# Kernel tuning notes

Hardware: AMD Instinct MI355X
Metric: run time of the kernel (lower is better)

Reference implementation:

```python
import jax, jax.numpy as jnp
import numpy as np

B, L, H, G = 16, 1024, 1024, 128


def setup_inputs() -> dict:
    key = jax.random.key(0)
    ks = jax.random.split(key, 6)
    s = 0.02
    return {
        "events": jax.random.normal(ks[0], (B, L, H), jnp.float32),
        "contexts": jax.random.normal(ks[1], (B, L - 1, H), jnp.float32),
        "Wzm": jax.random.normal(ks[2], (2 * H, G), jnp.float32) * s,
        "bzm": jnp.zeros((G,), jnp.float32),
        "Wzv": jax.random.normal(ks[3], (2 * H, G), jnp.float32) * s,
        "bzv": jnp.zeros((G,), jnp.float32),
        "Wqm": jax.random.normal(ks[4], (3 * H, G), jnp.float32) * s,
        "bqm": jnp.zeros((G,), jnp.float32),
        "Wqv": jax.random.normal(ks[5], (3 * H, G), jnp.float32) * s,
        "bqv": jnp.zeros((G,), jnp.float32),
    }


def reference(events, contexts, Wzm, bzm, Wzv, bzv, Wqm, bqm, Wqv, bqv):
    # adjacent event pairs: [B, L-1, 2H]
    ep = jnp.concatenate([events[:, :-1, :], events[:, 1:, :]], axis=-1)
    z_mean = ep @ Wzm + bzm          # [B, L-1, G]
    z_log_var = ep @ Wzv + bzv
    ce = jnp.concatenate([ep, contexts], axis=-1)  # [B, L-1, 3H]
    q_z_mean = ce @ Wqm + bqm
    q_z_log_var = ce @ Wqv + bqv
    # closed-form KL(p || q) for diagonal Gaussians, summed over G per (b, pair)
    kl = 0.5 * jnp.sum(
        q_z_log_var - z_log_var
        + (jnp.exp(z_log_var) + (z_mean - q_z_mean) ** 2) * jnp.exp(-q_z_log_var)
        - 1.0,
        axis=-1,
    )  # [B, L-1]
    kl_loss = jnp.mean(kl).reshape(1)  # sum over (b, pair) / (B * (L-1))
    return (z_mean, z_log_var, q_z_mean, q_z_log_var, kl_loss)
```

## Files before the change

kernel.cpp:

```cpp
#include <hip/hip_runtime.h>
#include <stdint.h>

typedef unsigned short u16;
typedef __attribute__((ext_vector_type(8))) short short8;
typedef __attribute__((ext_vector_type(4))) float f32x4;
typedef __attribute__((ext_vector_type(2))) uint32_t u32x2;

#define B_      16
#define L_      1024
#define H_      1024
#define G_      128
#define M_TOT   16368
#define K_TOT   3072
#define OUT_SEG 2095104
#define KL_IDX  (4*OUT_SEG)
#define KL_BLOCKS 4092

#define WS_WT_OFF    0
#define WS_BIAS_OFF  3145728
#define WS_PART_OFF  3147776

__device__ inline u16 f2bf(float f) {
    union { float f; uint32_t u; } x; x.f = f;
    uint32_t u = x.u;
    return (u16)((u + 0x7fffu + ((u >> 16) & 1u)) >> 16);
}

__device__ inline void gload16(const void* g, void* l) {
    __builtin_amdgcn_global_load_lds(
        (const __attribute__((address_space(1))) void*)g,
        (__attribute__((address_space(3))) void*)l, 16, 0, 0);
}

__global__ __launch_bounds__(256) void prep_kernel(
    const float* __restrict__ Wzm, const float* __restrict__ bzm,
    const float* __restrict__ Wzv, const float* __restrict__ bzv,
    const float* __restrict__ Wqm, const float* __restrict__ bqm,
    const float* __restrict__ Wqv, const float* __restrict__ bqv,
    u16* __restrict__ wt, float* __restrict__ bias)
{
    int n = blockIdx.x;
    int tid = threadIdx.x;
    const float* W; const float* bsrc; int g; int kmax;
    if (n < 128)      { W = Wzm; bsrc = bzm; g = n;       kmax = 2048; }
    else if (n < 256) { W = Wzv; bsrc = bzv; g = n - 128; kmax = 2048; }
    else if (n < 384) { W = Wqm; bsrc = bqm; g = n - 256; kmax = 3072; }
    else              { W = Wqv; bsrc = bqv; g = n - 384; kmax = 3072; }
    if (tid == 0) bias[n] = bsrc[g];
    #pragma unroll
    for (int i = 0; i < 12; ++i) {
        int k = i * 256 + tid;
        float v = (k < kmax) ? W[(size_t)k * G_ + g] : 0.0f;
        wt[(size_t)n * K_TOT + k] = f2bf(v);
    }
}

__global__ __launch_bounds__(512, 1) void gemm_kernel(
    const float* __restrict__ events, const float* __restrict__ contexts,
    const u16* __restrict__ wt, const float* __restrict__ bias,
    float* __restrict__ out)
{
    __shared__ u16 Ab[2][128 * 64];
    __shared__ u16 Bs[2][256 * 64];

    const int tid = threadIdx.x;
    const int bid = blockIdx.x;
    const int xx  = bid & 7;
    const int jj  = bid >> 3;
    const int nb  = jj & 1;
    const int mp  = (jj >> 1) * 8 + xx;
    const int m0  = mp * 128;

    const int lane = tid & 63;
    const int w    = tid >> 6;
    const int wm   = (w >> 2) * 64;
    const int wn   = (w & 3) * 64;
    const int lr   = lane & 15;
    const int kg   = lane >> 4;

    const int r = tid >> 2;
    const int q = tid & 3;
    int m = m0 + r; if (m > M_TOT - 1) m = M_TOT - 1;
    int bb = m / 1023;
    int tt = m - bb * 1023;
    const float* pa0 = events   + ((size_t)(bb * L_ + tt)) * H_;
    const float* pa2 = contexts + ((size_t)(bb * (L_ - 1) + tt)) * H_;
    int aw[4];
    #pragma unroll
    for (int j = 0; j < 4; ++j)
        aw[j] = r * 64 + (((2 * j + (q >> 1)) ^ (r & 7)) << 3) + (q & 1) * 4;

    const u16* bS[4];
    #pragma unroll
    for (int it = 0; it < 4; ++it) {
        int c  = it * 512 + tid;
        int v  = c >> 3;
        int cs = (c & 7) ^ (v & 7);
        bS[it] = wt + (size_t)(nb * 256 + v) * K_TOT + cs * 8;
    }

    int aoff[4][2], boff[4][2];
    #pragma unroll
    for (int i = 0; i < 4; ++i) {
        int row = wm + i * 16 + lr;
        int nn  = wn + i * 16 + lr;
        #pragma unroll
        for (int ks = 0; ks < 2; ++ks) {
            aoff[i][ks] = row * 64 + (((ks * 4 + kg) ^ (row & 7)) << 3);
            boff[i][ks] = nn  * 64 + (((ks * 4 + kg) ^ (nn  & 7)) << 3);
        }
    }

    f32x4 acc[4][4];
    #pragma unroll
    for (int i = 0; i < 4; ++i)
        #pragma unroll
        for (int j = 0; j < 4; ++j)
            acc[i][j] = (f32x4){0.f, 0.f, 0.f, 0.f};

    auto stageB = [&](int buf, int kt) {
        int k0 = kt * 64;
        #pragma unroll
        for (int it = 0; it < 4; ++it)
            gload16(bS[it] + k0, &Bs[buf][(it * 512 + tid) * 8]);
    };
    auto compute = [&](int buf) {
        #pragma unroll
        for (int ks = 0; ks < 2; ++ks) {
            short8 a[4], bf[4];
            #pragma unroll
            for (int i = 0; i < 4; ++i)
                a[i] = *(const short8*)&Ab[buf][aoff[i][ks]];
            #pragma unroll
            for (int j = 0; j < 4; ++j)
                bf[j] = *(const short8*)&Bs[buf][boff[j][ks]];
            __builtin_amdgcn_s_setprio(1);
            #pragma unroll
            for (int i = 0; i < 4; ++i)
                #pragma unroll
                for (int j = 0; j < 4; ++j)
                    acc[i][j] = __builtin_amdgcn_mfma_f32_16x16x32_bf16(
                        a[i], bf[j], acc[i][j], 0, 0, 0);
            __builtin_amdgcn_s_setprio(0);
        }
    };

    f32x4 P0, P1, P2, P3;
    f32x4 Q0, Q1, Q2, Q3;

#define LOADA(p, KT)                                                           \
    {                                                                          \
        int k0_ = (KT) * 64;                                                   \
        int rg_ = (KT) >> 4;                                                   \
        int kq_ = (k0_ & 1023) + q * 4;                                        \
        const float* s_ = (rg_ == 0) ? pa0 : (rg_ == 1 ? (pa0 + H_) : pa2);    \
        s_ += kq_;                                                             \
        p##0 = *(const f32x4*)(s_ +  0);                                       \
        p##1 = *(const f32x4*)(s_ + 16);                                       \
        p##2 = *(const f32x4*)(s_ + 32);                                       \
        p##3 = *(const f32x4*)(s_ + 48);                                       \
    }
#define CVT1(p, J, BUF)                                                        \
    {                                                                          \
        uint32_t lo_, hi_;                                                     \
        asm("v_cvt_pk_bf16_f32 %0, %1, %2" : "=v"(lo_) : "v"(p##J[0]), "v"(p##J[1])); \
        asm("v_cvt_pk_bf16_f32 %0, %1, %2" : "=v"(hi_) : "v"(p##J[2]), "v"(p##J[3])); \
        *(u32x2*)&Ab[BUF][aw[J]] = (u32x2){lo_, hi_};                          \
    }
#define CVTW(p, BUF)  CVT1(p, 0, BUF) CVT1(p, 1, BUF) CVT1(p, 2, BUF) CVT1(p, 3, BUF)

#define WAITV(N)                                                               \
    asm volatile("s_waitcnt vmcnt(" #N ")" ::: "memory");                      \
    __builtin_amdgcn_sched_barrier(0);
#define LGKM0                                                                  \
    asm volatile("s_waitcnt lgkmcnt(0)" ::: "memory");                         \
    __builtin_amdgcn_sched_barrier(0);
#define BAR __builtin_amdgcn_s_barrier()

    LOADA(P, 0);
    stageB(0, 0);
    WAITV(4);
    CVTW(P, 0);
    LOADA(Q, 1);
    LGKM0;

    for (int t = 0; t < 46; t += 2) {
        LOADA(P, t + 2);
        stageB(1, t + 1);
        WAITV(8); BAR;
        compute(0);
        CVTW(Q, 1);
        LGKM0; BAR;
        if (t + 3 < 48) LOADA(Q, t + 3);
        stageB(0, t + 2);
        WAITV(8); BAR;
        compute(1);
        CVTW(P, 0);
        LGKM0; BAR;
    }
    stageB(1, 47);
    WAITV(4); BAR;
    compute(0);
    CVTW(Q, 1);
    LGKM0; BAR;
    WAITV(0); BAR;
    compute(1);

#undef LOADA
#undef CVT1
#undef CVTW
#undef WAITV
#undef LGKM0
#undef BAR

    #pragma unroll
    for (int i = 0; i < 4; ++i) {
        int mloc = wm + i * 16 + kg * 4;
        #pragma unroll
        for (int j = 0; j < 4; ++j) {
            int gcol = nb * 256 + wn + j * 16 + lr;
            int seg  = gcol >> 7;
            int col  = gcol & 127;
            float bv = bias[gcol];
            float* obase = out + (size_t)seg * OUT_SEG + col;
            #pragma unroll
            for (int rr = 0; rr < 4; ++rr) {
                int mo = m0 + mloc + rr;
                if (mo < M_TOT) obase[(size_t)mo * G_] = acc[i][j][rr] + bv;
            }
        }
    }
}

__global__ __launch_bounds__(256) void kl_kernel(const float* __restrict__ out,
                                                 float* __restrict__ partial)
{
    int wid  = threadIdx.x >> 6;
    int row  = blockIdx.x * 4 + wid;
    int lane = threadIdx.x & 63;
    const float* zm  = out;
    const float* zlv = out + OUT_SEG;
    const float* qm  = out + (size_t)2 * OUT_SEG;
    const float* qlv = out + (size_t)3 * OUT_SEG;
    size_t base = (size_t)row * G_;
    float s = 0.f;
    #pragma unroll
    for (int hh = 0; hh < 2; ++hh) {
        int g = lane + hh * 64;
        float a = zm[base + g], b = zlv[base + g];
        float c = qm[base + g], d = qlv[base + g];
        float diff = a - c;
        s += d - b + (__expf(b) + diff * diff) * __expf(-d) - 1.0f;
    }
    #pragma unroll
    for (int off = 32; off > 0; off >>= 1)
        s += __shfl_down(s, off);
    __shared__ float pw[4];
    if (lane == 0) pw[wid] = s;
    __syncthreads();
    if (threadIdx.x == 0)
        partial[blockIdx.x] = pw[0] + pw[1] + pw[2] + pw[3];
}

__global__ __launch_bounds__(256) void kl_final(const float* __restrict__ partial,
                                                float* __restrict__ out)
{
    float s = 0.f;
    for (int i = threadIdx.x; i < KL_BLOCKS; i += 256) s += partial[i];
    #pragma unroll
    for (int off = 32; off > 0; off >>= 1)
        s += __shfl_down(s, off);
    __shared__ float pw[4];
    int wid = threadIdx.x >> 6;
    int lane = threadIdx.x & 63;
    if (lane == 0) pw[wid] = s;
    __syncthreads();
    if (threadIdx.x == 0)
        out[KL_IDX] = 0.5f * (pw[0] + pw[1] + pw[2] + pw[3]) / (float)M_TOT;
}

extern "C" void kernel_launch(void* const* d_in, const int* in_sizes, int n_in,
                              void* d_out, int out_size, void* d_ws, size_t ws_size,
                              hipStream_t stream)
{
    const float* events   = (const float*)d_in[0];
    const float* contexts = (const float*)d_in[1];
    const float* Wzm = (const float*)d_in[2];
    const float* bzm = (const float*)d_in[3];
    const float* Wzv = (const float*)d_in[4];
    const float* bzv = (const float*)d_in[5];
    const float* Wqm = (const float*)d_in[6];
    const float* bqm = (const float*)d_in[7];
    const float* Wqv = (const float*)d_in[8];
    const float* bqv = (const float*)d_in[9];
    float* out = (float*)d_out;

    u16*   wt      = (u16*)((char*)d_ws + WS_WT_OFF);
    float* bias    = (float*)((char*)d_ws + WS_BIAS_OFF);
    float* partial = (float*)((char*)d_ws + WS_PART_OFF);

    prep_kernel<<<512, 256, 0, stream>>>(Wzm, bzm, Wzv, bzv, Wqm, bqm, Wqv, bqv,
                                         wt, bias);
    gemm_kernel<<<256, 512, 0, stream>>>(events, contexts, wt, bias, out);
    kl_kernel<<<KL_BLOCKS, 256, 0, stream>>>(out, partial);
    kl_final<<<1, 256, 0, stream>>>(partial, out);
}
```

Before: 100.6 us.

## Retile GEMM to 128x128 blocks with 256 threads, two blocks per CU

The GEMM block tile shrinks from 128x256 (512 threads) to 128x128 (256 threads), launching 512 blocks with launch bounds allowing two blocks per CU. Each thread now loads and converts two A rows per k-step, and the vmcnt waits are raised to match. The goal is more resident blocks and better latency hiding, since 256 blocks may underfill the CUs. The cost is that each A tile is re-read and re-converted four times instead of twice, which doubles fp32 activation traffic, and register pressure rises.

```diff
diff --git a/kernel.cpp b/kernel.cpp
--- a/kernel.cpp
+++ b/kernel.cpp
@@ -55,48 +55,54 @@
     }
 }
 
-__global__ __launch_bounds__(512, 1) void gemm_kernel(
+__global__ __launch_bounds__(256, 2) void gemm_kernel(
     const float* __restrict__ events, const float* __restrict__ contexts,
     const u16* __restrict__ wt, const float* __restrict__ bias,
     float* __restrict__ out)
 {
     __shared__ u16 Ab[2][128 * 64];
-    __shared__ u16 Bs[2][256 * 64];
+    __shared__ u16 Bs[2][128 * 64];
 
     const int tid = threadIdx.x;
     const int bid = blockIdx.x;
     const int xx  = bid & 7;
     const int jj  = bid >> 3;
-    const int nb  = jj & 1;
-    const int mp  = (jj >> 1) * 8 + xx;
+    const int nb  = jj & 3;
+    const int mp  = (jj >> 2) * 8 + xx;
     const int m0  = mp * 128;
 
     const int lane = tid & 63;
     const int w    = tid >> 6;
-    const int wm   = (w >> 2) * 64;
-    const int wn   = (w & 3) * 64;
+    const int wm   = (w >> 1) * 64;
+    const int wn   = (w & 1) * 64;
     const int lr   = lane & 15;
     const int kg   = lane >> 4;
 
-    const int r = tid >> 2;
-    const int q = tid & 3;
-    int m = m0 + r; if (m > M_TOT - 1) m = M_TOT - 1;
-    int bb = m / 1023;
-    int tt = m - bb * 1023;
-    const float* pa0 = events   + ((size_t)(bb * L_ + tt)) * H_;
-    const float* pa2 = contexts + ((size_t)(bb * (L_ - 1) + tt)) * H_;
-    int aw[4];
-    #pragma unroll
-    for (int j = 0; j < 4; ++j)
-        aw[j] = r * 64 + (((2 * j + (q >> 1)) ^ (r & 7)) << 3) + (q & 1) * 4;
+    const int r0 = tid >> 2;
+    const int q  = tid & 3;
+    const float* paE[2]; const float* paC[2];
+    int aw[2][4];
+    #pragma unroll
+    for (int g = 0; g < 2; ++g) {
+        int r = r0 + g * 64;
+        int m = m0 + r; if (m > M_TOT - 1) m = M_TOT - 1;
+        int b = m / 1023;
+        int t = m - b * 1023;
+        paE[g] = events   + ((size_t)(b * L_ + t)) * H_;
+        paC[g] = contexts + ((size_t)(b * (L_ - 1) + t)) * H_;
+        #pragma unroll
+        for (int j = 0; j < 4; ++j)
+            aw[g][j] = r * 64 + (((2 * j + (q >> 1)) ^ (r & 7)) << 3)
+                     + (q & 1) * 4;
+    }
 
     const u16* bS[4];
     #pragma unroll
     for (int it = 0; it < 4; ++it) {
-        int c  = it * 512 + tid;
+        int c  = it * 256 + tid;
         int v  = c >> 3;
         int cs = (c & 7) ^ (v & 7);
-        bS[it] = wt + (size_t)(nb * 256 + v) * K_TOT + cs * 8;
+        bS[it] = wt + (size_t)(nb * 128 + v) * K_TOT + cs * 8;
     }
 
     int aoff[4][2], boff[4][2];
@@ -122,7 +128,7 @@
         int k0 = kt * 64;
         #pragma unroll
         for (int it = 0; it < 4; ++it)
-            gload16(bS[it] + k0, &Bs[buf][(it * 512 + tid) * 8]);
+            gload16(bS[it] + k0, &Bs[buf][(it * 256 + tid) * 8]);
     };
     auto compute = [&](int buf) {
         #pragma unroll
@@ -145,29 +151,40 @@
         }
     };
 
-    f32x4 P0, P1, P2, P3;
-    f32x4 Q0, Q1, Q2, Q3;
+    f32x4 P0, P1, P2, P3, P4, P5, P6, P7;
+    f32x4 Q0, Q1, Q2, Q3, Q4, Q5, Q6, Q7;
 
 #define LOADA(p, KT)                                                           \
     {                                                                          \
         int k0_ = (KT) * 64;                                                   \
         int rg_ = (KT) >> 4;                                                   \
         int kq_ = (k0_ & 1023) + q * 4;                                        \
-        const float* s_ = (rg_ == 0) ? pa0 : (rg_ == 1 ? (pa0 + H_) : pa2);    \
-        s_ += kq_;                                                             \
-        p##0 = *(const f32x4*)(s_ +  0);                                       \
-        p##1 = *(const f32x4*)(s_ + 16);                                       \
-        p##2 = *(const f32x4*)(s_ + 32);                                       \
-        p##3 = *(const f32x4*)(s_ + 48);                                       \
-    }
-#define CVT1(p, J, BUF)                                                        \
+        const float* s0_ = (rg_ == 0) ? paE[0]                                 \
+                          : (rg_ == 1 ? (paE[0] + H_) : paC[0]);               \
+        const float* s1_ = (rg_ == 0) ? paE[1]                                 \
+                          : (rg_ == 1 ? (paE[1] + H_) : paC[1]);               \
+        s0_ += kq_; s1_ += kq_;                                                \
+        p##0 = *(const f32x4*)(s0_ +  0);                                      \
+        p##1 = *(const f32x4*)(s0_ + 16);                                      \
+        p##2 = *(const f32x4*)(s0_ + 32);                                      \
+        p##3 = *(const f32x4*)(s0_ + 48);                                      \
+        p##4 = *(const f32x4*)(s1_ +  0);                                      \
+        p##5 = *(const f32x4*)(s1_ + 16);                                      \
+        p##6 = *(const f32x4*)(s1_ + 32);                                      \
+        p##7 = *(const f32x4*)(s1_ + 48);                                      \
+    }
+#define CVT1(p, RI, G, J, BUF)                                                 \
     {                                                                          \
         uint32_t lo_, hi_;                                                     \
-        asm("v_cvt_pk_bf16_f32 %0, %1, %2" : "=v"(lo_) : "v"(p##J[0]), "v"(p##J[1])); \
-        asm("v_cvt_pk_bf16_f32 %0, %1, %2" : "=v"(hi_) : "v"(p##J[2]), "v"(p##J[3])); \
-        *(u32x2*)&Ab[BUF][aw[J]] = (u32x2){lo_, hi_};                          \
-    }
-#define CVTW(p, BUF)  CVT1(p, 0, BUF) CVT1(p, 1, BUF) CVT1(p, 2, BUF) CVT1(p, 3, BUF)
+        asm("v_cvt_pk_bf16_f32 %0, %1, %2" : "=v"(lo_) : "v"(p##RI[0]), "v"(p##RI[1])); \
+        asm("v_cvt_pk_bf16_f32 %0, %1, %2" : "=v"(hi_) : "v"(p##RI[2]), "v"(p##RI[3])); \
+        *(u32x2*)&Ab[BUF][aw[G][J]] = (u32x2){lo_, hi_};                       \
+    }
+#define CVTW(p, BUF)                                                           \
+    CVT1(p, 0, 0, 0, BUF) CVT1(p, 1, 0, 1, BUF)                                \
+    CVT1(p, 2, 0, 2, BUF) CVT1(p, 3, 0, 3, BUF)                                \
+    CVT1(p, 4, 1, 0, BUF) CVT1(p, 5, 1, 1, BUF)                                \
+    CVT1(p, 6, 1, 2, BUF) CVT1(p, 7, 1, 3, BUF)
 
 #define WAITV(N)                                                               \
     asm volatile("s_waitcnt vmcnt(" #N ")" ::: "memory");                      \
@@ -187,13 +204,13 @@
     for (int t = 0; t < 46; t += 2) {
         LOADA(P, t + 2);
         stageB(1, t + 1);
-        WAITV(8); BAR;
+        WAITV(12); BAR;
         compute(0);
         CVTW(Q, 1);
         LGKM0; BAR;
-        if (t + 3 < 48) LOADA(Q, t + 3);
+        LOADA(Q, t + 3);
         stageB(0, t + 2);
-        WAITV(8); BAR;
+        WAITV(12); BAR;
         compute(1);
         CVTW(P, 0);
         LGKM0; BAR;
@@ -213,20 +230,19 @@
 #undef LGKM0
 #undef BAR
 
+    const float* bptr = bias + nb * 128;
+    float* obase = out + (size_t)nb * OUT_SEG;
     #pragma unroll
     for (int i = 0; i < 4; ++i) {
         int mloc = wm + i * 16 + kg * 4;
         #pragma unroll
         for (int j = 0; j < 4; ++j) {
-            int gcol = nb * 256 + wn + j * 16 + lr;
-            int seg  = gcol >> 7;
-            int col  = gcol & 127;
-            float bv = bias[gcol];
-            float* obase = out + (size_t)seg * OUT_SEG + col;
+            int g = wn + j * 16 + lr;
+            float bv = bptr[g];
             #pragma unroll
             for (int rr = 0; rr < 4; ++rr) {
                 int mo = m0 + mloc + rr;
-                if (mo < M_TOT) obase[(size_t)mo * G_] = acc[i][j][rr] + bv;
+                if (mo < M_TOT) obase[(size_t)mo * G_ + g] = acc[i][j][rr] + bv;
             }
         }
     }
@@ -301,7 +317,7 @@
 
     prep_kernel<<<512, 256, 0, stream>>>(Wzm, bzm, Wzv, bzv, Wqm, bqm, Wqv, bqv,
                                          wt, bias);
-    gemm_kernel<<<256, 512, 0, stream>>>(events, contexts, wt, bias, out);
+    gemm_kernel<<<512, 256, 0, stream>>>(events, contexts, wt, bias, out);
     kl_kernel<<<KL_BLOCKS, 256, 0, stream>>>(out, partial);
     kl_final<<<1, 256, 0, stream>>>(partial, out);
 }
```

Result: faster. 96.19 us (-4.4%).
